# Performance work log

Measured on AMD Instinct MI355X. Metric: run time of the kernel, lower is better.

Reference implementation:

```python
import jax, jax.numpy as jnp
import numpy as np

N = 50000
E = 800000
IN_DIM = 128
HID = 32
HEADS = 4
NEG_SLOPE = 0.2


def setup_inputs() -> dict:
    key = jax.random.key(0)
    ks = jax.random.split(key, 12)
    x = jax.random.normal(ks[0], (N, IN_DIM), dtype=jnp.float32)
    edge_index = jax.random.randint(ks[1], (2, E), 0, N, dtype=jnp.int64)
    s1 = 1.0 / np.sqrt(IN_DIM)
    s2 = 1.0 / np.sqrt(HEADS * HID)
    W1 = jax.random.normal(ks[2], (IN_DIM, HEADS * HID), dtype=jnp.float32) * s1
    a_src1 = jax.random.normal(ks[3], (HEADS, HID), dtype=jnp.float32) * s1
    a_dst1 = jax.random.normal(ks[4], (HEADS, HID), dtype=jnp.float32) * s1
    b1 = jnp.zeros((HEADS * HID,), dtype=jnp.float32)
    W2 = jax.random.normal(ks[5], (HEADS * HID, HID), dtype=jnp.float32) * s2
    a_src2 = jax.random.normal(ks[6], (1, HID), dtype=jnp.float32) * s2
    a_dst2 = jax.random.normal(ks[7], (1, HID), dtype=jnp.float32) * s2
    b2 = jnp.zeros((HID,), dtype=jnp.float32)
    return {"x": x, "edge_index": edge_index, "W1": W1, "a_src1": a_src1,
            "a_dst1": a_dst1, "b1": b1, "W2": W2, "a_src2": a_src2,
            "a_dst2": a_dst2, "b2": b2}


def _gat_layer(x, W, a_src, a_dst, bias, src, dst, heads, ch):
    n = x.shape[0]
    h = (x @ W).reshape(n, heads, ch)                    # [N,H,C]
    # per-node attention halves (GATv1): a_src . h_i, a_dst . h_j
    al_s = jnp.einsum('nhc,hc->nh', h, a_src)            # [N,H]
    al_d = jnp.einsum('nhc,hc->nh', h, a_dst)
    e = jax.nn.leaky_relu(al_s[src] + al_d[dst], NEG_SLOPE)  # [E,H]
    # segment softmax over edges sharing the same destination
    e_max = jax.ops.segment_max(e, dst, num_segments=n)
    e_exp = jnp.exp(e - e_max[dst])
    denom = jax.ops.segment_sum(e_exp, dst, num_segments=n)
    alpha = e_exp / (denom[dst] + 1e-16)                 # [E,H]
    msg = h[src] * alpha[:, :, None]                     # [E,H,C]
    out = jax.ops.segment_sum(msg, dst, num_segments=n)  # [N,H,C]
    return out.reshape(n, heads * ch) + bias


def reference(x, edge_index, W1, a_src1, a_dst1, b1, W2, a_src2, a_dst2, b2):
    n = x.shape[0]
    # PyG GATConv adds self-loops by default
    loops = jnp.arange(n, dtype=edge_index.dtype)
    src = jnp.concatenate([edge_index[0], loops])
    dst = jnp.concatenate([edge_index[1], loops])
    h = _gat_layer(x, W1, a_src1, a_dst1, b1, src, dst, HEADS, HID)
    h = jax.nn.elu(h)
    out = _gat_layer(h, W2, a_src2, a_dst2, b2, src, dst, 1, HID)
    return out
```

## Files before the change

### kernel.cpp

```cpp
#include <hip/hip_runtime.h>
#include <hip/hip_bf16.h>

#define NN 50000
#define EE 800000
#define EN (EE + NN)
#define IN_DIM 128
#define HID 32
#define HEADS 4
#define F1 (HEADS * HID)
#define NEG 0.2f
#define SLOT 64

typedef __hip_bfloat16 bf16;
typedef __bf16 bf16x8 __attribute__((ext_vector_type(8)));
typedef float f32x4 __attribute__((ext_vector_type(4)));

__device__ __forceinline__ float cvt(float v) { return v; }
__device__ __forceinline__ float cvt(bf16 v)  { return __bfloat162float(v); }

__device__ __forceinline__ float bflo(unsigned u) {
    union { unsigned u; float f; } v; v.u = u << 16; return v.f;
}
__device__ __forceinline__ float bfhi(unsigned u) {
    union { unsigned u; float f; } v; v.u = u & 0xFFFF0000u; return v.f;
}

__device__ __forceinline__ unsigned short f2bf_bits(float f) {
    union { float f; unsigned u; } v; v.f = f;
    unsigned r = v.u + 0x7FFFu + ((v.u >> 16) & 1u);
    return (unsigned short)(r >> 16);
}

__device__ __forceinline__ unsigned short f2h_bits(float f) {
    _Float16 h = (_Float16)f;
    union { _Float16 h; unsigned short s; } v; v.h = h; return v.s;
}
__device__ __forceinline__ float h2f(unsigned short s) {
    union { _Float16 h; unsigned short s; } v; v.s = s; return (float)v.h;
}

#define ZERO_B ((NN + 255) / 256)
#define PREP_B (1 + ZERO_B + 16 + 1)

__global__ void k_prep(const void* xv, const void* eiv,
                       const void* W1v, const void* W2v,
                       int* __restrict__ flags, int* __restrict__ counts,
                       unsigned short* __restrict__ W1T,
                       unsigned short* __restrict__ W2T) {
    const int b = blockIdx.x, t = threadIdx.x;
    if (b == 0) {
        if (t < 64) {
            const unsigned* xw = (const unsigned*)xv;
            const unsigned* ew = (const unsigned*)eiv;
            int lo_nz = 0, huge = 0, hi_nz = 0;
            for (int j = 0; j < 4; ++j) {
                unsigned w = xw[t * 4 + j];
                unsigned lo = w & 0xFFFFu;
                if (lo != 0u) lo_nz = 1;
                if (((lo >> 7) & 0xFFu) >= 0xC0u) huge = 1;
                unsigned eo = ew[(t * 4 + j) * 2 + 1];
                if (eo != 0u) hi_nz = 1;
            }
            unsigned long long m_lo = __ballot(lo_nz);
            unsigned long long m_hg = __ballot(huge);
            unsigned long long m_hi = __ballot(hi_nz);
            if (t == 0) {
                flags[0] = (m_lo == 0ull || m_hg != 0ull) ? 1 : 0;
                flags[1] = (m_hi == 0ull) ? 1 : 0;
            }
        }
        return;
    }
    if (b <= ZERO_B) {
        int i = (b - 1) * 256 + t;
        if (i < NN) counts[i] = 0;
        return;
    }
    __shared__ int sf;
    if (t < 64) {
        const unsigned* xw = (const unsigned*)xv;
        int lo_nz = 0, huge = 0;
        for (int j = 0; j < 4; ++j) {
            unsigned w = xw[t * 4 + j];
            unsigned lo = w & 0xFFFFu;
            if (lo != 0u) lo_nz = 1;
            if (((lo >> 7) & 0xFFu) >= 0xC0u) huge = 1;
        }
        unsigned long long m_lo = __ballot(lo_nz);
        unsigned long long m_hg = __ballot(huge);
        if (t == 0) sf = (m_lo == 0ull || m_hg != 0ull) ? 1 : 0;
    }
    __syncthreads();
    const int f32in = sf;
    const int tb = b - 1 - ZERO_B;
    if (tb < 16) {
        const unsigned short* wg = (const unsigned short*)W1v;
        const float* wf = (const float*)W1v;
        for (int i = 0; i < 4; ++i) {
            int j = tb * 1024 + i * 256 + t;
            int k = j >> 7, n = j & 127;
            W1T[n * 128 + k] = f32in ? f2bf_bits(wf[j]) : wg[j];
        }
    } else {
        const unsigned short* wg = (const unsigned short*)W2v;
        const float* wf = (const float*)W2v;
        for (int i = 0; i < 16; ++i) {
            int j = i * 256 + t;
            int k = j >> 5, n = j & 31;
            W2T[n * 128 + k] = f32in ? f2bf_bits(wf[j]) : wg[j];
        }
    }
}

#define PAIR_B ((EN / 2 + 255) / 256)

__global__ void k_hist(const void* ei, const int* __restrict__ flags,
                       int* __restrict__ counts, int* __restrict__ rank) {
    int p = blockIdx.x * 256 + threadIdx.x;
    int i2 = p * 2;
    if (i2 >= EN) return;
    int d0, d1;
    if (i2 >= EE) { d0 = i2 - EE; d1 = d0 + 1; }
    else if (flags[1]) {
        const long long* e64 = (const long long*)ei;
        long2 dd = *(const long2*)&e64[EE + i2];
        d0 = (int)dd.x; d1 = (int)dd.y;
    } else {
        const int* e32 = (const int*)ei;
        int2 dd = *(const int2*)&e32[EE + i2];
        d0 = dd.x; d1 = dd.y;
    }
    int r0 = atomicAdd(&counts[d0], 1);
    int r1 = atomicAdd(&counts[d1], 1);
    *(int2*)&rank[i2] = make_int2(r0, r1);
}

__global__ void k_scatter(const void* ei, const int* __restrict__ flags,
                          const int* __restrict__ rank, int* __restrict__ srcs2) {
    int p = blockIdx.x * 256 + threadIdx.x;
    int i2 = p * 2;
    if (i2 >= EN) return;
    int s0, s1, d0, d1;
    if (i2 >= EE) { s0 = d0 = i2 - EE; s1 = d1 = s0 + 1; }
    else if (flags[1]) {
        const long long* e64 = (const long long*)ei;
        long2 ss = *(const long2*)&e64[i2];
        long2 dd = *(const long2*)&e64[EE + i2];
        s0 = (int)ss.x; s1 = (int)ss.y; d0 = (int)dd.x; d1 = (int)dd.y;
    } else {
        const int* e32 = (const int*)ei;
        int2 ss = *(const int2*)&e32[i2];
        int2 dd = *(const int2*)&e32[EE + i2];
        s0 = ss.x; s1 = ss.y; d0 = dd.x; d1 = dd.y;
    }
    int2 rr = *(const int2*)&rank[i2];
    if (rr.x < SLOT) srcs2[d0 * SLOT + rr.x] = s0;
    if (rr.y < SLOT) srcs2[d1 * SLOT + rr.y] = s1;
}

#define MROWS 64
#define LDK 136

__global__ __launch_bounds__(256) void k_lin1_mfma(
    const void* xv, const unsigned short* __restrict__ W1T,
    const void* as1v, const void* ad1v,
    const int* __restrict__ flags, unsigned* __restrict__ h1,
    float* __restrict__ als, float* __restrict__ ald)
{
    __shared__ __align__(16) char smem[(MROWS + 128) * LDK * 2];
    unsigned short* xs  = (unsigned short*)smem;
    unsigned short* w1t = xs + MROWS * LDK;
    float* hs = (float*)smem;
    __shared__ float sa[F1], sd[F1];

    const int t = threadIdx.x;
    const int row0 = blockIdx.x * MROWS;
    const int f32in = flags[0];

    if (t < F1) {
        sa[t] = f32in ? ((const float*)as1v)[t] : cvt(((const bf16*)as1v)[t]);
        sd[t] = f32in ? ((const float*)ad1v)[t] : cvt(((const bf16*)ad1v)[t]);
    }
    if (!f32in) {
        const uint4* xg = (const uint4*)xv;
        for (int i = 0; i < 4; ++i) {
            int id = i * 256 + t;
            int m = id >> 4, seg = id & 15;
            int gr = row0 + m;
            uint4 val = (gr < NN) ? xg[(size_t)gr * 16 + seg] : make_uint4(0, 0, 0, 0);
            *(uint4*)&xs[m * LDK + seg * 8] = val;
        }
    } else {
        const float4* xf = (const float4*)xv;
        for (int i = 0; i < 8; ++i) {
            int id = i * 256 + t;
            int m = id >> 5, c = id & 31;
            int gr = row0 + m;
            float4 v = (gr < NN) ? xf[(size_t)gr * 32 + c]
                                 : make_float4(0.f, 0.f, 0.f, 0.f);
            unsigned w0 = (unsigned)f2bf_bits(v.x) | ((unsigned)f2bf_bits(v.y) << 16);
            unsigned w1 = (unsigned)f2bf_bits(v.z) | ((unsigned)f2bf_bits(v.w) << 16);
            *(uint2*)&xs[m * LDK + c * 4] = make_uint2(w0, w1);
        }
    }
    {
        const uint4* wg = (const uint4*)W1T;
        for (int i = 0; i < 8; ++i) {
            int id = i * 256 + t;
            int n = id >> 4, seg = id & 15;
            *(uint4*)&w1t[n * LDK + seg * 8] = wg[id];
        }
    }
    __syncthreads();

    const int wave = t >> 6, lane = t & 63, quad = lane >> 4, l16 = lane & 15;
    f32x4 acc[8];
#pragma unroll
    for (int ni = 0; ni < 8; ++ni) acc[ni] = (f32x4){0.f, 0.f, 0.f, 0.f};

    const int arow = wave * 16 + l16;
#pragma unroll
    for (int kc = 0; kc < 4; ++kc) {
        int ko = kc * 32 + quad * 8;
        bf16x8 av = *(const bf16x8*)&xs[arow * LDK + ko];
#pragma unroll
        for (int ni = 0; ni < 8; ++ni) {
            bf16x8 bv = *(const bf16x8*)&w1t[(ni * 16 + l16) * LDK + ko];
            acc[ni] = __builtin_amdgcn_mfma_f32_16x16x32_bf16(av, bv, acc[ni], 0, 0, 0);
        }
    }
    __syncthreads();

#pragma unroll
    for (int ni = 0; ni < 8; ++ni)
#pragma unroll
        for (int r = 0; r < 4; ++r) {
            int m = wave * 16 + quad * 4 + r;
            hs[m * 132 + ni * 16 + l16] = acc[ni][r];
        }
    __syncthreads();

    for (int i = 0; i < 16; ++i) {
        int id = i * 256 + t;
        int m = id >> 6, wd = id & 63;
        int gr = row0 + m;
        if (gr < NN) {
            unsigned pw = (unsigned)f2bf_bits(hs[m * 132 + 2 * wd]) |
                          ((unsigned)f2bf_bits(hs[m * 132 + 2 * wd + 1]) << 16);
            h1[(size_t)gr * 64 + wd] = pw;
        }
    }
    {
        int m = t >> 2, h = t & 3;
        int gr = row0 + m;
        if (gr < NN) {
            float ps = 0.f, pd = 0.f;
#pragma unroll
            for (int jj = 0; jj < 32; ++jj) {
                int j = (jj + 8 * h) & 31;
                float v = hs[m * 132 + h * 32 + j];
                ps += v * sa[h * 32 + j];
                pd += v * sd[h * 32 + j];
            }
            als[gr * 4 + h] = ps;
            ald[gr * 4 + h] = pd;
        }
    }
}

__global__ __launch_bounds__(256) void k_agg1(
    const int* __restrict__ counts, const int* __restrict__ srcs2,
    const float* __restrict__ als, const float* __restrict__ ald,
    const bf16* __restrict__ h1, const void* b1v, const int* __restrict__ flags,
    uint4* __restrict__ hm)
{
    const int lane = threadIdx.x & 63;
    const int d = blockIdx.x * 4 + (threadIdx.x >> 6);
    const int q = lane >> 4;
    const int u = lane & 15;
    const int h = u >> 2;
    const int start = d * SLOT;
    const int end = start + min(counts[d], SLOT);
    const uint4* rows = (const uint4*)h1;
    const float advh = ald[d * 4 + h];

    float A[8] = {0,0,0,0,0,0,0,0}, B[8] = {0,0,0,0,0,0,0,0};
    float DA = 0.f, DB = 0.f;
    int e = start + q;
    for (; e + 4 < end; e += 8) {
        int s0 = srcs2[e], s1 = srcs2[e + 4];
        float e0 = als[s0 * 4 + h] + advh;
        float e1 = als[s1 * 4 + h] + advh;
        e0 = e0 > 0.f ? e0 : NEG * e0;
        e1 = e1 > 0.f ? e1 : NEG * e1;
        float x0 = __expf(e0), x1 = __expf(e1);
        uint4 u0 = rows[(size_t)s0 * 16 + u];
        uint4 u1 = rows[(size_t)s1 * 16 + u];
        A[0] += x0 * bflo(u0.x); A[1] += x0 * bfhi(u0.x);
        A[2] += x0 * bflo(u0.y); A[3] += x0 * bfhi(u0.y);
        A[4] += x0 * bflo(u0.z); A[5] += x0 * bfhi(u0.z);
        A[6] += x0 * bflo(u0.w); A[7] += x0 * bfhi(u0.w); DA += x0;
        B[0] += x1 * bflo(u1.x); B[1] += x1 * bfhi(u1.x);
        B[2] += x1 * bflo(u1.y); B[3] += x1 * bfhi(u1.y);
        B[4] += x1 * bflo(u1.z); B[5] += x1 * bfhi(u1.z);
        B[6] += x1 * bflo(u1.w); B[7] += x1 * bfhi(u1.w); DB += x1;
    }
    for (; e < end; e += 4) {
        int s0 = srcs2[e];
        float e0 = als[s0 * 4 + h] + advh;
        e0 = e0 > 0.f ? e0 : NEG * e0;
        float x0 = __expf(e0);
        uint4 u0 = rows[(size_t)s0 * 16 + u];
        A[0] += x0 * bflo(u0.x); A[1] += x0 * bfhi(u0.x);
        A[2] += x0 * bflo(u0.y); A[3] += x0 * bfhi(u0.y);
        A[4] += x0 * bflo(u0.z); A[5] += x0 * bfhi(u0.z);
        A[6] += x0 * bflo(u0.w); A[7] += x0 * bfhi(u0.w); DA += x0;
    }
    float a[8];
#pragma unroll
    for (int j = 0; j < 8; ++j) a[j] = A[j] + B[j];
    float dsum = DA + DB;
#pragma unroll
    for (int j = 0; j < 8; ++j) {
        a[j] += __shfl_xor(a[j], 16);
        a[j] += __shfl_xor(a[j], 32);
    }
    dsum += __shfl_xor(dsum, 16);
    dsum += __shfl_xor(dsum, 32);
    if (q == 0) {
        float inv = 1.f / (dsum + 1e-16f);
        float bb[8];
        if (flags[0]) {
            float4 b0 = ((const float4*)b1v)[2 * u];
            float4 b1 = ((const float4*)b1v)[2 * u + 1];
            bb[0] = b0.x; bb[1] = b0.y; bb[2] = b0.z; bb[3] = b0.w;
            bb[4] = b1.x; bb[5] = b1.y; bb[6] = b1.z; bb[7] = b1.w;
        } else {
            uint4 ub = ((const uint4*)b1v)[u];
            bb[0] = bflo(ub.x); bb[1] = bfhi(ub.x); bb[2] = bflo(ub.y); bb[3] = bfhi(ub.y);
            bb[4] = bflo(ub.z); bb[5] = bfhi(ub.z); bb[6] = bflo(ub.w); bb[7] = bfhi(ub.w);
        }
        float v[8];
#pragma unroll
        for (int j = 0; j < 8; ++j) {
            float vv = a[j] * inv + bb[j];
            v[j] = vv > 0.f ? vv : (__expf(vv) - 1.f);
        }
        uint4 w;
        w.x = (unsigned)f2bf_bits(v[0]) | ((unsigned)f2bf_bits(v[1]) << 16);
        w.y = (unsigned)f2bf_bits(v[2]) | ((unsigned)f2bf_bits(v[3]) << 16);
        w.z = (unsigned)f2bf_bits(v[4]) | ((unsigned)f2bf_bits(v[5]) << 16);
        w.w = (unsigned)f2bf_bits(v[6]) | ((unsigned)f2bf_bits(v[7]) << 16);
        hm[(size_t)d * 16 + u] = w;
    }
}

__global__ __launch_bounds__(256) void k_mid_mfma(
    const bf16* __restrict__ hm, const unsigned short* __restrict__ W2T,
    const void* as2v, const void* ad2v,
    const int* __restrict__ flags, unsigned short* __restrict__ h2,
    float* __restrict__ als2, float* __restrict__ ald2)
{
    __shared__ __align__(16) unsigned short hs[MROWS * LDK];
    __shared__ __align__(16) unsigned short w2t[32 * LDK];
    __shared__ float sa2[HID], sd2[HID];

    const int t = threadIdx.x;
    const int row0 = blockIdx.x * MROWS;
    const int f32in = flags[0];

    if (t < HID) {
        sa2[t] = f32in ? ((const float*)as2v)[t] : cvt(((const bf16*)as2v)[t]);
        sd2[t] = f32in ? ((const float*)ad2v)[t] : cvt(((const bf16*)ad2v)[t]);
    }
    {
        const uint4* hg = (const uint4*)hm;
        for (int i = 0; i < 4; ++i) {
            int id = i * 256 + t;
            int m = id >> 4, seg = id & 15;
            int gr = row0 + m;
            uint4 val = (gr < NN) ? hg[(size_t)gr * 16 + seg] : make_uint4(0, 0, 0, 0);
            *(uint4*)&hs[m * LDK + seg * 8] = val;
        }
        const uint4* wg = (const uint4*)W2T;
        for (int i = 0; i < 2; ++i) {
            int id = i * 256 + t;
            int n = id >> 4, seg = id & 15;
            *(uint4*)&w2t[n * LDK + seg * 8] = wg[id];
        }
    }
    __syncthreads();

    const int wave = t >> 6, lane = t & 63, quad = lane >> 4, l16 = lane & 15;
    f32x4 acc[2];
    acc[0] = (f32x4){0.f, 0.f, 0.f, 0.f};
    acc[1] = (f32x4){0.f, 0.f, 0.f, 0.f};
    const int arow = wave * 16 + l16;
#pragma unroll
    for (int kc = 0; kc < 4; ++kc) {
        int ko = kc * 32 + quad * 8;
        bf16x8 av = *(const bf16x8*)&hs[arow * LDK + ko];
#pragma unroll
        for (int ni = 0; ni < 2; ++ni) {
            bf16x8 bv = *(const bf16x8*)&w2t[(ni * 16 + l16) * LDK + ko];
            acc[ni] = __builtin_amdgcn_mfma_f32_16x16x32_bf16(av, bv, acc[ni], 0, 0, 0);
        }
    }

#pragma unroll
    for (int ni = 0; ni < 2; ++ni)
#pragma unroll
        for (int r = 0; r < 4; ++r) {
            int gr = row0 + wave * 16 + quad * 4 + r;
            if (gr < NN) h2[(size_t)gr * 32 + ni * 16 + l16] = f2h_bits(acc[ni][r]);
        }

    float ps[4], pd[4];
#pragma unroll
    for (int r = 0; r < 4; ++r) {
        ps[r] = acc[0][r] * sa2[l16] + acc[1][r] * sa2[16 + l16];
        pd[r] = acc[0][r] * sd2[l16] + acc[1][r] * sd2[16 + l16];
    }
#pragma unroll
    for (int mask = 1; mask < 16; mask <<= 1)
#pragma unroll
        for (int r = 0; r < 4; ++r) {
            ps[r] += __shfl_xor(ps[r], mask);
            pd[r] += __shfl_xor(pd[r], mask);
        }
    if (l16 == 0) {
#pragma unroll
        for (int r = 0; r < 4; ++r) {
            int gr = row0 + wave * 16 + quad * 4 + r;
            if (gr < NN) { als2[gr] = ps[r]; ald2[gr] = pd[r]; }
        }
    }
}

__global__ __launch_bounds__(256) void k_agg2(
    const int* __restrict__ counts, const int* __restrict__ srcs2,
    const float* __restrict__ als2, const float* __restrict__ ald2,
    const uint2* __restrict__ h2,
    const void* b2v, const int* __restrict__ flags, void* out)
{
    const int lane = threadIdx.x & 63;
    const int node = blockIdx.x * 4 + (threadIdx.x >> 6);
    const int q = lane >> 3;
    const int u = lane & 7;
    const int start = node * SLOT;
    const int end = start + min(counts[node], SLOT);
    const float adv = ald2[node];

    float A0 = 0.f, A1 = 0.f, A2 = 0.f, A3 = 0.f, D0 = 0.f;
    for (int e = start + q; e < end; e += 8) {
        int s0 = srcs2[e];
        float e0 = als2[s0] + adv;
        e0 = e0 > 0.f ? e0 : NEG * e0;
        float x0 = __expf(e0);
        uint2 w = h2[(size_t)s0 * 8 + u];
        A0 += x0 * h2f((unsigned short)(w.x & 0xFFFFu));
        A1 += x0 * h2f((unsigned short)(w.x >> 16));
        A2 += x0 * h2f((unsigned short)(w.y & 0xFFFFu));
        A3 += x0 * h2f((unsigned short)(w.y >> 16));
        D0 += x0;
    }
    A0 += __shfl_xor(A0, 8);  A1 += __shfl_xor(A1, 8);
    A2 += __shfl_xor(A2, 8);  A3 += __shfl_xor(A3, 8);  D0 += __shfl_xor(D0, 8);
    A0 += __shfl_xor(A0, 16); A1 += __shfl_xor(A1, 16);
    A2 += __shfl_xor(A2, 16); A3 += __shfl_xor(A3, 16); D0 += __shfl_xor(D0, 16);
    A0 += __shfl_xor(A0, 32); A1 += __shfl_xor(A1, 32);
    A2 += __shfl_xor(A2, 32); A3 += __shfl_xor(A3, 32); D0 += __shfl_xor(D0, 32);
    if (q == 0) {
        float inv = 1.f / (D0 + 1e-16f);
        float r0 = A0 * inv, r1 = A1 * inv, r2 = A2 * inv, r3 = A3 * inv;
        if (flags[0]) {
            float4 bb = ((const float4*)b2v)[u];
            ((float4*)out)[(size_t)node * 8 + u] =
                make_float4(r0 + bb.x, r1 + bb.y, r2 + bb.z, r3 + bb.w);
        } else {
            uint2 ub = ((const uint2*)b2v)[u];
            r0 += bflo(ub.x); r1 += bfhi(ub.x); r2 += bflo(ub.y); r3 += bfhi(ub.y);
            unsigned w0 = (unsigned)f2bf_bits(r0) | ((unsigned)f2bf_bits(r1) << 16);
            unsigned w1 = (unsigned)f2bf_bits(r2) | ((unsigned)f2bf_bits(r3) << 16);
            ((uint2*)out)[(size_t)node * 8 + u] = make_uint2(w0, w1);
        }
    }
}

extern "C" void kernel_launch(void* const* d_in, const int* in_sizes, int n_in,
                              void* d_out, int out_size, void* d_ws, size_t ws_size,
                              hipStream_t stream) {
    const void* x    = d_in[0];
    const void* ei   = d_in[1];
    const void* W1   = d_in[2];
    const void* a_s1 = d_in[3];
    const void* a_d1 = d_in[4];
    const void* b1   = d_in[5];
    const void* W2   = d_in[6];
    const void* a_s2 = d_in[7];
    const void* a_d2 = d_in[8];
    const void* b2v  = d_in[9];

    int*   flags  = (int*)d_ws;
    char*  pc     = (char*)d_ws + 256;
    uint4* hm     = (uint4*)pc;            pc += (size_t)NN * 16 * 16;
    int*   rank   = (int*)hm;
    bf16*  h1     = (bf16*)pc;             pc += (size_t)NN * F1 * 2;
    unsigned short* h2 = (unsigned short*)h1;
    int*   srcs2  = (int*)pc;              pc += (size_t)NN * SLOT * 4;
    float* al_s1  = (float*)pc;            pc += (size_t)NN * HEADS * 4;
    float* al_d1  = (float*)pc;            pc += (size_t)NN * HEADS * 4;
    float* al_s2  = (float*)pc;            pc += (size_t)NN * 4;
    float* al_d2  = (float*)pc;            pc += (size_t)NN * 4;
    int*   counts = (int*)pc;              pc += (size_t)NN * 4;
    unsigned short* W1T = (unsigned short*)pc; pc += (size_t)128 * 128 * 2;
    unsigned short* W2T = (unsigned short*)pc; pc += (size_t)32 * 128 * 2;

    k_prep<<<PREP_B, 256, 0, stream>>>(x, ei, W1, W2, flags, counts, W1T, W2T);
    k_hist<<<PAIR_B, 256, 0, stream>>>(ei, flags, counts, rank);
    k_scatter<<<PAIR_B, 256, 0, stream>>>(ei, flags, rank, srcs2);
    k_lin1_mfma<<<(NN + MROWS - 1) / MROWS, 256, 0, stream>>>(x, W1T, a_s1, a_d1,
                                                              flags, (unsigned*)h1,
                                                              al_s1, al_d1);
    k_agg1<<<NN / 4, 256, 0, stream>>>(counts, srcs2, al_s1, al_d1, h1, b1,
                                       flags, hm);
    k_mid_mfma<<<(NN + MROWS - 1) / MROWS, 256, 0, stream>>>((const bf16*)hm, W2T, a_s2,
                                                             a_d2, flags, h2, al_s2, al_d2);
    k_agg2<<<NN / 4, 256, 0, stream>>>(counts, srcs2, al_s2, al_d2,
                                       (const uint2*)h2, b2v, flags, d_out);
}
```

Measured before the change: 220.6 us.

## Merge edge scatter into lin1 kernel launch and precompute slot indices in hist

The histogram kernel now reads both source and destination, computes each edge's final slot address and stores (slot, src) pairs. The separate scatter kernel is removed: its work runs in extra blocks appended to the lin1 MFMA kernel's grid, so the scatter overlaps the dense matmul and one launch is saved. The cost is that the sr buffer doubles in size (int4 per edge pair) and the hist kernel does more loads. The scatter blocks also still reserve the large static shared memory of the MFMA blocks, which can limit occupancy.

```diff
diff --git a/kernel.cpp b/kernel.cpp
--- a/kernel.cpp
+++ b/kernel.cpp
@@ -115,28 +115,7 @@
 #define PAIR_B ((EN / 2 + 255) / 256)
 
 __global__ void k_hist(const void* ei, const int* __restrict__ flags,
-                       int* __restrict__ counts, int* __restrict__ rank) {
-    int p = blockIdx.x * 256 + threadIdx.x;
-    int i2 = p * 2;
-    if (i2 >= EN) return;
-    int d0, d1;
-    if (i2 >= EE) { d0 = i2 - EE; d1 = d0 + 1; }
-    else if (flags[1]) {
-        const long long* e64 = (const long long*)ei;
-        long2 dd = *(const long2*)&e64[EE + i2];
-        d0 = (int)dd.x; d1 = (int)dd.y;
-    } else {
-        const int* e32 = (const int*)ei;
-        int2 dd = *(const int2*)&e32[EE + i2];
-        d0 = dd.x; d1 = dd.y;
-    }
-    int r0 = atomicAdd(&counts[d0], 1);
-    int r1 = atomicAdd(&counts[d1], 1);
-    *(int2*)&rank[i2] = make_int2(r0, r1);
-}
-
-__global__ void k_scatter(const void* ei, const int* __restrict__ flags,
-                          const int* __restrict__ rank, int* __restrict__ srcs2) {
+                       int* __restrict__ counts, int* __restrict__ sr) {
     int p = blockIdx.x * 256 + threadIdx.x;
     int i2 = p * 2;
     if (i2 >= EN) return;
@@ -153,20 +132,35 @@
         int2 dd = *(const int2*)&e32[EE + i2];
         s0 = ss.x; s1 = ss.y; d0 = dd.x; d1 = dd.y;
     }
-    int2 rr = *(const int2*)&rank[i2];
-    if (rr.x < SLOT) srcs2[d0 * SLOT + rr.x] = s0;
-    if (rr.y < SLOT) srcs2[d1 * SLOT + rr.y] = s1;
+    int r0 = atomicAdd(&counts[d0], 1);
+    int r1 = atomicAdd(&counts[d1], 1);
+    int slot0 = (r0 < SLOT) ? d0 * SLOT + r0 : -1;
+    int slot1 = (r1 < SLOT) ? d1 * SLOT + r1 : -1;
+    *(int4*)&sr[i2 * 2] = make_int4(slot0, s0, slot1, s1);
 }
 
 #define MROWS 64
 #define LDK 136
-
-__global__ __launch_bounds__(256) void k_lin1_mfma(
+#define LIN_B ((NN + MROWS - 1) / MROWS)
+#define FUSE_B (LIN_B + PAIR_B)
+
+__global__ __launch_bounds__(256) void k_fused(
     const void* xv, const unsigned short* __restrict__ W1T,
     const void* as1v, const void* ad1v,
-    const int* __restrict__ flags, unsigned* __restrict__ h1,
+    const int* __restrict__ flags, const int* __restrict__ sr,
+    int* __restrict__ srcs2, unsigned* __restrict__ h1,
     float* __restrict__ als, float* __restrict__ ald)
 {
+    if (blockIdx.x >= LIN_B) {
+        int p = (blockIdx.x - LIN_B) * 256 + threadIdx.x;
+        int i2 = p * 2;
+        if (i2 >= EN) return;
+        int4 v = *(const int4*)&sr[i2 * 2];
+        if (v.x >= 0) srcs2[v.x] = v.y;
+        if (v.z >= 0) srcs2[v.z] = v.w;
+        return;
+    }
+
     __shared__ __align__(16) char smem[(MROWS + 128) * LDK * 2];
     unsigned short* xs  = (unsigned short*)smem;
     unsigned short* w1t = xs + MROWS * LDK;
@@ -504,7 +498,7 @@
     int*   flags  = (int*)d_ws;
     char*  pc     = (char*)d_ws + 256;
     uint4* hm     = (uint4*)pc;            pc += (size_t)NN * 16 * 16;
-    int*   rank   = (int*)hm;
+    int*   sr     = (int*)hm;
     bf16*  h1     = (bf16*)pc;             pc += (size_t)NN * F1 * 2;
     unsigned short* h2 = (unsigned short*)h1;
     int*   srcs2  = (int*)pc;              pc += (size_t)NN * SLOT * 4;
@@ -517,11 +511,9 @@
     unsigned short* W2T = (unsigned short*)pc; pc += (size_t)32 * 128 * 2;
 
     k_prep<<<PREP_B, 256, 0, stream>>>(x, ei, W1, W2, flags, counts, W1T, W2T);
-    k_hist<<<PAIR_B, 256, 0, stream>>>(ei, flags, counts, rank);
-    k_scatter<<<PAIR_B, 256, 0, stream>>>(ei, flags, rank, srcs2);
-    k_lin1_mfma<<<(NN + MROWS - 1) / MROWS, 256, 0, stream>>>(x, W1T, a_s1, a_d1,
-                                                              flags, (unsigned*)h1,
-                                                              al_s1, al_d1);
+    k_hist<<<PAIR_B, 256, 0, stream>>>(ei, flags, counts, sr);
+    k_fused<<<FUSE_B, 256, 0, stream>>>(x, W1T, a_s1, a_d1, flags, sr, srcs2,
+                                        (unsigned*)h1, al_s1, al_d1);
     k_agg1<<<NN / 4, 256, 0, stream>>>(counts, srcs2, al_s1, al_d1, h1, b1,
                                        flags, hm);
     k_mid_mfma<<<(NN + MROWS - 1) / MROWS, 256, 0, stream>>>((const bf16*)hm, W2T, a_s2,
```

Result: faster. 215.0 us (-2.5%).
